# Kernel tuning notes

Measured on AMD Instinct MI355X. Metric: run time of the kernel, lower is better.

The kernel has to match this reference:

```python
import jax, jax.numpy as jnp
import numpy as np

N_NODES = 50000


def gcn_conv(x, src, dst, W, b):
    """PyG GCNConv: symmetric-normalized aggregation with self-loops.
    out[i] = sum_{j->i} deg^{-1/2}[j] deg^{-1/2}[i] (x_j @ W) + b
    src/dst already include self-loop edges.
    """
    n = x.shape[0]
    ew = jnp.ones(src.shape[0], dtype=x.dtype)
    deg = jax.ops.segment_sum(ew, dst, num_segments=n)  # [N]
    dinv = jnp.where(deg > 0, jax.lax.rsqrt(deg), 0.0).astype(x.dtype)
    norm = dinv[src] * dinv[dst]  # [E+N]
    xw = x @ W  # [N, z] dense transform first (as PyG does)
    msg = xw[src] * norm[:, None]  # gather + scale, [E+N, z]
    out = jax.ops.segment_sum(msg, dst, num_segments=n)  # scatter-add
    return out + b


def prelu(x, a):
    return jnp.where(x > 0, x, a * x)


def setup_inputs() -> dict:
    key = jax.random.key(0)
    k1, k2, k3, k4 = jax.random.split(key, 4)
    in_dim = z_dim = 96
    n_edges = 800000
    x = jax.random.normal(k1, (N_NODES, in_dim), dtype=jnp.float32)
    edge_index = jax.random.randint(k2, (2, n_edges), 0, N_NODES, dtype=jnp.int32)
    # Glorot-style init for GCN weights
    s1 = 1.0 / np.sqrt(in_dim)
    W1 = jax.random.uniform(k3, (in_dim, z_dim), jnp.float32, -s1, s1)
    W2 = jax.random.uniform(k4, (z_dim, z_dim), jnp.float32, -s1, s1)
    b1 = jnp.zeros((z_dim,), jnp.float32)
    b2 = jnp.zeros((z_dim,), jnp.float32)
    prelu_a = jnp.full((z_dim,), 0.25, jnp.float32)  # shared PReLU, per-channel
    return {"x": x, "edge_index": edge_index, "W1": W1, "b1": b1,
            "W2": W2, "b2": b2, "prelu_a": prelu_a}


def reference(x, edge_index, W1, b1, W2, b2, prelu_a):
    n = x.shape[0]
    loop = jnp.arange(n, dtype=edge_index.dtype)
    src = jnp.concatenate([edge_index[0], loop])
    dst = jnp.concatenate([edge_index[1], loop])
    h = prelu(gcn_conv(x, src, dst, W1, b1), prelu_a)
    h = prelu(gcn_conv(h, src, dst, W2, b2), prelu_a)
    return h
```

## Files before the change

### kernel.cpp

```cpp
#include <hip/hip_runtime.h>
#include <hip/hip_fp16.h>

#define D 96
#define D4 24
#define MAXBINS 256
#define CAP 16384

static inline size_t alignup(size_t x) { return (x + 255) & ~size_t(255); }

__device__ inline float4 f4fma(float s, float4 a, float4 acc) {
    acc.x = fmaf(s, a.x, acc.x);
    acc.y = fmaf(s, a.y, acc.y);
    acc.z = fmaf(s, a.z, acc.z);
    acc.w = fmaf(s, a.w, acc.w);
    return acc;
}

__device__ inline void u2add(uint2 rv, float4& a) {
    __half2 h0 = *reinterpret_cast<__half2*>(&rv.x);
    __half2 h1 = *reinterpret_cast<__half2*>(&rv.y);
    float2 f0 = __half22float2(h0);
    float2 f1 = __half22float2(h1);
    a.x += f0.x; a.y += f0.y; a.z += f1.x; a.w += f1.y;
}

__global__ __launch_bounds__(256) void init_kernel(int* __restrict__ cursor) {
    cursor[threadIdx.x] = (int)threadIdx.x * CAP;
}

__global__ __launch_bounds__(1024) void dist_kernel(const int* __restrict__ src,
                                                    const int* __restrict__ dst, int E,
                                                    int* __restrict__ cursor,
                                                    int* __restrict__ ebuf) {
    __shared__ int h[MAXBINS];
    __shared__ int base[MAXBINS];
    const int tid = threadIdx.x;
    if (tid < MAXBINS) h[tid] = 0;
    __syncthreads();
    const int e0 = blockIdx.x * 4096 + tid;
    int pk[4], bn[4], rk[4];
    bool val[4];
    #pragma unroll
    for (int q = 0; q < 4; ++q) {
        int e = e0 + q * 1024;
        val[q] = e < E;
        if (val[q]) {
            int s = src[e], d = dst[e];
            bn[q] = d >> 8;
            pk[q] = ((d & 255) << 16) | s;
            rk[q] = atomicAdd(&h[bn[q]], 1);
        }
    }
    __syncthreads();
    if (tid < MAXBINS && h[tid]) base[tid] = atomicAdd(&cursor[tid], h[tid]);
    __syncthreads();
    #pragma unroll
    for (int q = 0; q < 4; ++q)
        if (val[q]) ebuf[base[bn[q]] + rk[q]] = pk[q];
}

__global__ __launch_bounds__(256) void bucketAB_kernel(const int* __restrict__ ebuf,
                                                       const int* __restrict__ cursor,
                                                       float* __restrict__ dinv,
                                                       int2* __restrict__ rowspan,
                                                       int* __restrict__ csr, int n) {
    __shared__ int cnt[256];
    __shared__ int cur[256];
    __shared__ int wsum[4];
    const int k = blockIdx.x;
    const int tid = threadIdx.x;
    const int bstart = k * CAP;
    const int bend = cursor[k];
    cnt[tid] = 0;
    __syncthreads();
    for (int e = bstart + tid; e < bend; e += 256)
        atomicAdd(&cnt[(ebuf[e] >> 16) & 255], 1);
    __syncthreads();
    int v = cnt[tid];
    const int lane = tid & 63, wid = tid >> 6;
    int sc = v;
    #pragma unroll
    for (int off = 1; off < 64; off <<= 1) {
        int t = __shfl_up(sc, off);
        if (lane >= off) sc += t;
    }
    if (lane == 63) wsum[wid] = sc;
    __syncthreads();
    int wprefix = 0;
    #pragma unroll
    for (int w = 0; w < 4; ++w)
        if (w < wid) wprefix += wsum[w];
    int mybase = bstart + wprefix + (sc - v);
    int node = k * 256 + tid;
    if (node < n) {
        dinv[node] = rsqrtf((float)(v + 1));
        rowspan[node] = make_int2(mybase, mybase + v);
    }
    cur[tid] = mybase;
    __syncthreads();
    for (int e = bstart + tid; e < bend; e += 256) {
        int pe = ebuf[e];
        int pos = atomicAdd(&cur[(pe >> 16) & 255], 1);
        csr[pos] = pe & 0xFFFF;
    }
}


__global__ __launch_bounds__(192) void matmul_kernel(const float* __restrict__ X,
                                                     const float* __restrict__ W,
                                                     const float* __restrict__ dinv,
                                                     uint2* __restrict__ Y, int n) {
    __shared__ float XsT[96 * 64];
    const int t = threadIdx.x;
    const int y = threadIdx.y;
    const int tid = y * 24 + t;
    const int row0 = blockIdx.x * 64;
    const float4* X4 = (const float4*)X;

    for (int i = tid; i < 64 * 24; i += 192) {
        int r = i / 24, c4 = i % 24;
        float4 v = make_float4(0.f, 0.f, 0.f, 0.f);
        if (row0 + r < n) v = X4[(size_t)(row0 + r) * D4 + c4];
        int rs = r ^ ((c4 & 15) << 2);
        XsT[(c4 * 4 + 0) * 64 + rs] = v.x;
        XsT[(c4 * 4 + 1) * 64 + rs] = v.y;
        XsT[(c4 * 4 + 2) * 64 + rs] = v.z;
        XsT[(c4 * 4 + 3) * 64 + rs] = v.w;
    }
    __syncthreads();

    const float4* W4 = (const float4*)W;
    float4 acc[8];
    #pragma unroll
    for (int r = 0; r < 8; ++r) acc[r] = make_float4(0.f, 0.f, 0.f, 0.f);
    const int rbase = y * 8;

    #pragma unroll 8
    for (int k = 0; k < 96; ++k) {
        float4 w = W4[k * D4 + t];
        int base0 = (rbase ^ (((k >> 2) & 15) << 2));
        float4 xa = *(const float4*)&XsT[k * 64 + base0];
        float4 xb = *(const float4*)&XsT[k * 64 + (base0 ^ 4)];
        acc[0] = f4fma(xa.x, w, acc[0]);
        acc[1] = f4fma(xa.y, w, acc[1]);
        acc[2] = f4fma(xa.z, w, acc[2]);
        acc[3] = f4fma(xa.w, w, acc[3]);
        acc[4] = f4fma(xb.x, w, acc[4]);
        acc[5] = f4fma(xb.y, w, acc[5]);
        acc[6] = f4fma(xb.z, w, acc[6]);
        acc[7] = f4fma(xb.w, w, acc[7]);
    }

    #pragma unroll
    for (int r = 0; r < 8; ++r) {
        int row = row0 + rbase + r;
        if (row < n) {
            float sc = dinv[row];
            __half2 ha = __float22half2_rn(make_float2(sc * acc[r].x, sc * acc[r].y));
            __half2 hb = __float22half2_rn(make_float2(sc * acc[r].z, sc * acc[r].w));
            uint2 st;
            st.x = *reinterpret_cast<unsigned int*>(&ha);
            st.y = *reinterpret_cast<unsigned int*>(&hb);
            Y[(size_t)row * D4 + t] = st;
        }
    }
}

__global__ __launch_bounds__(384) void aggregate_kernel(const uint2* __restrict__ XH,
                                                        const int* __restrict__ csr,
                                                        const int2* __restrict__ rowspan,
                                                        const float* __restrict__ dinv,
                                                        const float4* __restrict__ b4,
                                                        const float4* __restrict__ pa4,
                                                        float4* __restrict__ out4, int n) {
    const int i = blockIdx.x * 16 + threadIdx.y;
    const int t = threadIdx.x;
    if (i >= n) return;
    const int2 be = rowspan[i];
    float4 a = make_float4(0.f, 0.f, 0.f, 0.f);
    int p = be.x;
    const int end = be.y;
    for (; p + 8 <= end; p += 8) {
        int s0 = csr[p + 0];
        int s1 = csr[p + 1];
        int s2 = csr[p + 2];
        int s3 = csr[p + 3];
        int s4 = csr[p + 4];
        int s5 = csr[p + 5];
        int s6 = csr[p + 6];
        int s7 = csr[p + 7];
        uint2 r0 = XH[(size_t)s0 * D4 + t];
        uint2 r1 = XH[(size_t)s1 * D4 + t];
        uint2 r2 = XH[(size_t)s2 * D4 + t];
        uint2 r3 = XH[(size_t)s3 * D4 + t];
        uint2 r4 = XH[(size_t)s4 * D4 + t];
        uint2 r5 = XH[(size_t)s5 * D4 + t];
        uint2 r6 = XH[(size_t)s6 * D4 + t];
        uint2 r7 = XH[(size_t)s7 * D4 + t];
        u2add(r0, a); u2add(r1, a); u2add(r2, a); u2add(r3, a);
        u2add(r4, a); u2add(r5, a); u2add(r6, a); u2add(r7, a);
    }
    if (p + 4 <= end) {
        int s0 = csr[p + 0];
        int s1 = csr[p + 1];
        int s2 = csr[p + 2];
        int s3 = csr[p + 3];
        uint2 r0 = XH[(size_t)s0 * D4 + t];
        uint2 r1 = XH[(size_t)s1 * D4 + t];
        uint2 r2 = XH[(size_t)s2 * D4 + t];
        uint2 r3 = XH[(size_t)s3 * D4 + t];
        u2add(r0, a); u2add(r1, a); u2add(r2, a); u2add(r3, a);
        p += 4;
    }
    for (; p < end; ++p)
        u2add(XH[(size_t)csr[p] * D4 + t], a);
    u2add(XH[(size_t)i * D4 + t], a);
    const float di = dinv[i];
    float4 b = b4[t], q = pa4[t];
    float4 v;
    v.x = fmaf(di, a.x, b.x);
    v.y = fmaf(di, a.y, b.y);
    v.z = fmaf(di, a.z, b.z);
    v.w = fmaf(di, a.w, b.w);
    v.x = v.x > 0.f ? v.x : q.x * v.x;
    v.y = v.y > 0.f ? v.y : q.y * v.y;
    v.z = v.z > 0.f ? v.z : q.z * v.z;
    v.w = v.w > 0.f ? v.w : q.w * v.w;
    out4[(size_t)i * D4 + t] = v;
}

extern "C" void kernel_launch(void* const* d_in, const int* in_sizes, int n_in,
                              void* d_out, int out_size, void* d_ws, size_t ws_size,
                              hipStream_t stream) {
    const float* x   = (const float*)d_in[0];
    const int*   ei  = (const int*)d_in[1];
    const float* W1  = (const float*)d_in[2];
    const float* b1  = (const float*)d_in[3];
    const float* W2  = (const float*)d_in[4];
    const float* b2  = (const float*)d_in[5];
    const float* pa  = (const float*)d_in[6];
    const int n = in_sizes[0] / D;
    const int E = in_sizes[1] / 2;
    const int* srcp = ei;
    const int* dstp = ei + E;

    const int nbins = (n + 255) / 256;
    const int nblk  = (E + 4095) / 4096;

    char* w = (char*)d_ws;
    int*   cursor  = (int*)w;    w += alignup(256 * 4);
    int*   ebuf    = (int*)w;    w += alignup((size_t)nbins * CAP * 4);
    int*   csr     = (int*)w;    w += alignup((size_t)nbins * CAP * 4);
    float* dinv    = (float*)w;  w += alignup((size_t)n * 4);
    int2*  rowspan = (int2*)w;   w += alignup((size_t)n * 8);
    uint2* xw      = (uint2*)w;  w += alignup((size_t)n * D * 2);
    float* out     = (float*)d_out;

    init_kernel<<<1, 256, 0, stream>>>(cursor);
    dist_kernel<<<nblk, 1024, 0, stream>>>(srcp, dstp, E, cursor, ebuf);
    bucketAB_kernel<<<nbins, 256, 0, stream>>>(ebuf, cursor, dinv, rowspan, csr, n);

    dim3 mblk(24, 8);
    const int mgrid = (n + 63) / 64;
    dim3 ablk(24, 16);
    const int agrid = (n + 15) / 16;

    matmul_kernel<<<mgrid, mblk, 0, stream>>>(x, W1, dinv, xw, n);
    aggregate_kernel<<<agrid, ablk, 0, stream>>>(xw, csr, rowspan, dinv,
                                                 (const float4*)b1, (const float4*)pa, (float4*)out, n);
    matmul_kernel<<<mgrid, mblk, 0, stream>>>(out, W2, dinv, xw, n);
    aggregate_kernel<<<agrid, ablk, 0, stream>>>(xw, csr, rowspan, dinv,
                                                 (const float4*)b2, (const float4*)pa, (float4*)out, n);
}
```

Measured before the change: 136.0 us.

## Split fp16 transformed features into three column planes for gather locality

The matmul now writes its fp16 output as three feature planes of 32 columns each, and aggregation launches separate blocks per plane with 8-thread rows and 48 nodes per block. Each plane's gather working set is a third the size, aiming to improve cache hit rate during the irregular neighbor gather. In exchange, the CSR indices and row spans are read three times, and each gathered row segment is only 64 bytes.

```diff
diff --git a/kernel.cpp b/kernel.cpp
--- a/kernel.cpp
+++ b/kernel.cpp
@@ -151,6 +151,7 @@
         acc[7] = f4fma(xb.w, w, acc[7]);
     }
 
+    const int plane = t >> 3, tp = t & 7;
     #pragma unroll
     for (int r = 0; r < 8; ++r) {
         int row = row0 + rbase + r;
@@ -161,7 +162,7 @@
             uint2 st;
             st.x = *reinterpret_cast<unsigned int*>(&ha);
             st.y = *reinterpret_cast<unsigned int*>(&hb);
-            Y[(size_t)row * D4 + t] = st;
+            Y[(size_t)plane * n * 8 + (size_t)row * 8 + tp] = st;
         }
     }
 }
@@ -172,61 +173,66 @@
                                                         const float* __restrict__ dinv,
                                                         const float4* __restrict__ b4,
                                                         const float4* __restrict__ pa4,
-                                                        float4* __restrict__ out4, int n) {
-    const int i = blockIdx.x * 16 + threadIdx.y;
+                                                        float4* __restrict__ out4,
+                                                        int n, int PB) {
+    const int p = blockIdx.x / PB;
+    const int vb = blockIdx.x - p * PB;
+    const int i = vb * 48 + threadIdx.y;
     const int t = threadIdx.x;
     if (i >= n) return;
+    const uint2* XP = XH + (size_t)p * n * 8;
     const int2 be = rowspan[i];
     float4 a = make_float4(0.f, 0.f, 0.f, 0.f);
-    int p = be.x;
+    int q = be.x;
     const int end = be.y;
-    for (; p + 8 <= end; p += 8) {
-        int s0 = csr[p + 0];
-        int s1 = csr[p + 1];
-        int s2 = csr[p + 2];
-        int s3 = csr[p + 3];
-        int s4 = csr[p + 4];
-        int s5 = csr[p + 5];
-        int s6 = csr[p + 6];
-        int s7 = csr[p + 7];
-        uint2 r0 = XH[(size_t)s0 * D4 + t];
-        uint2 r1 = XH[(size_t)s1 * D4 + t];
-        uint2 r2 = XH[(size_t)s2 * D4 + t];
-        uint2 r3 = XH[(size_t)s3 * D4 + t];
-        uint2 r4 = XH[(size_t)s4 * D4 + t];
-        uint2 r5 = XH[(size_t)s5 * D4 + t];
-        uint2 r6 = XH[(size_t)s6 * D4 + t];
-        uint2 r7 = XH[(size_t)s7 * D4 + t];
+    for (; q + 8 <= end; q += 8) {
+        int s0 = csr[q + 0];
+        int s1 = csr[q + 1];
+        int s2 = csr[q + 2];
+        int s3 = csr[q + 3];
+        int s4 = csr[q + 4];
+        int s5 = csr[q + 5];
+        int s6 = csr[q + 6];
+        int s7 = csr[q + 7];
+        uint2 r0 = XP[(size_t)s0 * 8 + t];
+        uint2 r1 = XP[(size_t)s1 * 8 + t];
+        uint2 r2 = XP[(size_t)s2 * 8 + t];
+        uint2 r3 = XP[(size_t)s3 * 8 + t];
+        uint2 r4 = XP[(size_t)s4 * 8 + t];
+        uint2 r5 = XP[(size_t)s5 * 8 + t];
+        uint2 r6 = XP[(size_t)s6 * 8 + t];
+        uint2 r7 = XP[(size_t)s7 * 8 + t];
         u2add(r0, a); u2add(r1, a); u2add(r2, a); u2add(r3, a);
         u2add(r4, a); u2add(r5, a); u2add(r6, a); u2add(r7, a);
     }
-    if (p + 4 <= end) {
-        int s0 = csr[p + 0];
-        int s1 = csr[p + 1];
-        int s2 = csr[p + 2];
-        int s3 = csr[p + 3];
-        uint2 r0 = XH[(size_t)s0 * D4 + t];
-        uint2 r1 = XH[(size_t)s1 * D4 + t];
-        uint2 r2 = XH[(size_t)s2 * D4 + t];
-        uint2 r3 = XH[(size_t)s3 * D4 + t];
+    if (q + 4 <= end) {
+        int s0 = csr[q + 0];
+        int s1 = csr[q + 1];
+        int s2 = csr[q + 2];
+        int s3 = csr[q + 3];
+        uint2 r0 = XP[(size_t)s0 * 8 + t];
+        uint2 r1 = XP[(size_t)s1 * 8 + t];
+        uint2 r2 = XP[(size_t)s2 * 8 + t];
+        uint2 r3 = XP[(size_t)s3 * 8 + t];
         u2add(r0, a); u2add(r1, a); u2add(r2, a); u2add(r3, a);
-        p += 4;
-    }
-    for (; p < end; ++p)
-        u2add(XH[(size_t)csr[p] * D4 + t], a);
-    u2add(XH[(size_t)i * D4 + t], a);
+        q += 4;
+    }
+    for (; q < end; ++q)
+        u2add(XP[(size_t)csr[q] * 8 + t], a);
+    u2add(XP[(size_t)i * 8 + t], a);
     const float di = dinv[i];
-    float4 b = b4[t], q = pa4[t];
+    const int c4 = p * 8 + t;
+    float4 b = b4[c4], qq = pa4[c4];
     float4 v;
     v.x = fmaf(di, a.x, b.x);
     v.y = fmaf(di, a.y, b.y);
     v.z = fmaf(di, a.z, b.z);
     v.w = fmaf(di, a.w, b.w);
-    v.x = v.x > 0.f ? v.x : q.x * v.x;
-    v.y = v.y > 0.f ? v.y : q.y * v.y;
-    v.z = v.z > 0.f ? v.z : q.z * v.z;
-    v.w = v.w > 0.f ? v.w : q.w * v.w;
-    out4[(size_t)i * D4 + t] = v;
+    v.x = v.x > 0.f ? v.x : qq.x * v.x;
+    v.y = v.y > 0.f ? v.y : qq.y * v.y;
+    v.z = v.z > 0.f ? v.z : qq.z * v.z;
+    v.w = v.w > 0.f ? v.w : qq.w * v.w;
+    out4[(size_t)i * D4 + c4] = v;
 }
 
 extern "C" void kernel_launch(void* const* d_in, const int* in_sizes, int n_in,
@@ -262,13 +268,16 @@
 
     dim3 mblk(24, 8);
     const int mgrid = (n + 63) / 64;
-    dim3 ablk(24, 16);
-    const int agrid = (n + 15) / 16;
+    dim3 ablk(8, 48);
+    const int PB = (n + 47) / 48;
+    const int agrid = 3 * PB;
 
     matmul_kernel<<<mgrid, mblk, 0, stream>>>(x, W1, dinv, xw, n);
     aggregate_kernel<<<agrid, ablk, 0, stream>>>(xw, csr, rowspan, dinv,
-                                                 (const float4*)b1, (const float4*)pa, (float4*)out, n);
+                                                 (const float4*)b1, (const float4*)pa,
+                                                 (float4*)out, n, PB);
     matmul_kernel<<<mgrid, mblk, 0, stream>>>(out, W2, dinv, xw, n);
     aggregate_kernel<<<agrid, ablk, 0, stream>>>(xw, csr, rowspan, dinv,
-                                                 (const float4*)b2, (const float4*)pa, (float4*)out, n);
-}
+                                                 (const float4*)b2, (const float4*)pa,
+                                                 (float4*)out, n, PB);
+}
```

After: 137.5 us. About the same (+1.1%).

## Fuse layer-1 aggregation with layer-2 dense transform in one kernel

Applied to the files above, without the earlier changes.

Replaces the layer-1 aggregate kernel and the following layer-2 matmul kernel with a single kernel. Each row's PReLU output is written to shared memory, multiplied by W2 staged in shared memory, and stored as scaled fp16 into a second buffer. This removes the fp32 intermediate write/read and one launch. In exchange, every block reloads the 36KB W2 into LDS, which may lower occupancy, and the per-row matmul reuses W2 less than the tiled matmul did.

```diff
diff --git a/kernel.cpp b/kernel.cpp
--- a/kernel.cpp
+++ b/kernel.cpp
@@ -22,6 +22,15 @@
     float2 f0 = __half22float2(h0);
     float2 f1 = __half22float2(h1);
     a.x += f0.x; a.y += f0.y; a.z += f1.x; a.w += f1.y;
+}
+
+__device__ inline uint2 packh4(float sc, float4 v) {
+    __half2 ha = __float22half2_rn(make_float2(sc * v.x, sc * v.y));
+    __half2 hb = __float22half2_rn(make_float2(sc * v.z, sc * v.w));
+    uint2 st;
+    st.x = *reinterpret_cast<unsigned int*>(&ha);
+    st.y = *reinterpret_cast<unsigned int*>(&hb);
+    return st;
 }
 
 __global__ __launch_bounds__(256) void init_kernel(int* __restrict__ cursor) {
@@ -154,29 +163,13 @@
     #pragma unroll
     for (int r = 0; r < 8; ++r) {
         int row = row0 + rbase + r;
-        if (row < n) {
-            float sc = dinv[row];
-            __half2 ha = __float22half2_rn(make_float2(sc * acc[r].x, sc * acc[r].y));
-            __half2 hb = __float22half2_rn(make_float2(sc * acc[r].z, sc * acc[r].w));
-            uint2 st;
-            st.x = *reinterpret_cast<unsigned int*>(&ha);
-            st.y = *reinterpret_cast<unsigned int*>(&hb);
-            Y[(size_t)row * D4 + t] = st;
-        }
-    }
-}
-
-__global__ __launch_bounds__(384) void aggregate_kernel(const uint2* __restrict__ XH,
-                                                        const int* __restrict__ csr,
-                                                        const int2* __restrict__ rowspan,
-                                                        const float* __restrict__ dinv,
-                                                        const float4* __restrict__ b4,
-                                                        const float4* __restrict__ pa4,
-                                                        float4* __restrict__ out4, int n) {
-    const int i = blockIdx.x * 16 + threadIdx.y;
-    const int t = threadIdx.x;
-    if (i >= n) return;
-    const int2 be = rowspan[i];
+        if (row < n) Y[(size_t)row * D4 + t] = packh4(dinv[row], acc[r]);
+    }
+}
+
+__device__ inline float4 gather_row(const uint2* __restrict__ XH,
+                                    const int* __restrict__ csr,
+                                    int2 be, int i, int t) {
     float4 a = make_float4(0.f, 0.f, 0.f, 0.f);
     int p = be.x;
     const int end = be.y;
@@ -215,6 +208,65 @@
     for (; p < end; ++p)
         u2add(XH[(size_t)csr[p] * D4 + t], a);
     u2add(XH[(size_t)i * D4 + t], a);
+    return a;
+}
+
+__global__ __launch_bounds__(384) void agg_mm_kernel(const uint2* __restrict__ XH,
+                                                     const int* __restrict__ csr,
+                                                     const int2* __restrict__ rowspan,
+                                                     const float* __restrict__ dinv,
+                                                     const float4* __restrict__ b4,
+                                                     const float4* __restrict__ pa4,
+                                                     const float* __restrict__ W2,
+                                                     uint2* __restrict__ Y, int n) {
+    __shared__ float4 W2s[96 * 24];
+    __shared__ float hbuf[16][96];
+    const int t = threadIdx.x;
+    const int y = threadIdx.y;
+    const int tid = y * 24 + t;
+    const int i = blockIdx.x * 16 + y;
+    const bool live = i < n;
+
+    const float4* W24 = (const float4*)W2;
+    for (int idx = tid; idx < 96 * 24; idx += 384) W2s[idx] = W24[idx];
+
+    float di = 1.f;
+    if (live) {
+        di = dinv[i];
+        float4 a = gather_row(XH, csr, rowspan[i], i, t);
+        float4 b = b4[t], q = pa4[t];
+        float4 v;
+        v.x = fmaf(di, a.x, b.x);
+        v.y = fmaf(di, a.y, b.y);
+        v.z = fmaf(di, a.z, b.z);
+        v.w = fmaf(di, a.w, b.w);
+        v.x = v.x > 0.f ? v.x : q.x * v.x;
+        v.y = v.y > 0.f ? v.y : q.y * v.y;
+        v.z = v.z > 0.f ? v.z : q.z * v.z;
+        v.w = v.w > 0.f ? v.w : q.w * v.w;
+        *(float4*)&hbuf[y][4 * t] = v;
+    }
+    __syncthreads();
+
+    float4 acc = make_float4(0.f, 0.f, 0.f, 0.f);
+    #pragma unroll 8
+    for (int k = 0; k < 96; ++k)
+        acc = f4fma(hbuf[y][k], W2s[k * 24 + t], acc);
+
+    if (live) Y[(size_t)i * D4 + t] = packh4(di, acc);
+}
+
+__global__ __launch_bounds__(384) void aggregate_kernel(const uint2* __restrict__ XH,
+                                                        const int* __restrict__ csr,
+                                                        const int2* __restrict__ rowspan,
+                                                        const float* __restrict__ dinv,
+                                                        const float4* __restrict__ b4,
+                                                        const float4* __restrict__ pa4,
+                                                        float4* __restrict__ out4, int n) {
+    const int i = blockIdx.x * 16 + threadIdx.y;
+    const int t = threadIdx.x;
+    if (i >= n) return;
+    float4 a = gather_row(XH, csr, rowspan[i], i, t);
     const float di = dinv[i];
     float4 b = b4[t], q = pa4[t];
     float4 v;
@@ -254,6 +306,7 @@
     float* dinv    = (float*)w;  w += alignup((size_t)n * 4);
     int2*  rowspan = (int2*)w;   w += alignup((size_t)n * 8);
     uint2* xw      = (uint2*)w;  w += alignup((size_t)n * D * 2);
+    uint2* xw2     = (uint2*)w;  w += alignup((size_t)n * D * 2);
     float* out     = (float*)d_out;
 
     init_kernel<<<1, 256, 0, stream>>>(cursor);
@@ -266,9 +319,10 @@
     const int agrid = (n + 15) / 16;
 
     matmul_kernel<<<mgrid, mblk, 0, stream>>>(x, W1, dinv, xw, n);
-    aggregate_kernel<<<agrid, ablk, 0, stream>>>(xw, csr, rowspan, dinv,
-                                                 (const float4*)b1, (const float4*)pa, (float4*)out, n);
-    matmul_kernel<<<mgrid, mblk, 0, stream>>>(out, W2, dinv, xw, n);
-    aggregate_kernel<<<agrid, ablk, 0, stream>>>(xw, csr, rowspan, dinv,
-                                                 (const float4*)b2, (const float4*)pa, (float4*)out, n);
-}
+    agg_mm_kernel<<<agrid, ablk, 0, stream>>>(xw, csr, rowspan, dinv,
+                                              (const float4*)b1, (const float4*)pa,
+                                              W2, xw2, n);
+    aggregate_kernel<<<agrid, ablk, 0, stream>>>(xw2, csr, rowspan, dinv,
+                                                 (const float4*)b2, (const float4*)pa,
+                                                 (float4*)out, n);
+}
```

After: 143.8 us. 1.06x slower.
